# Kernel optimization log

Hardware: AMD Instinct MI355X
Metric: run time of the kernel (lower is better)

Reference implementation:

```python
import jax, jax.numpy as jnp
import numpy as np

N = 50000
E = 400000
D = 128

def _linear(v, W, b):
    return v @ W + b

def setup_inputs() -> dict:
    key = jax.random.key(0)
    ks = jax.random.split(key, 24)
    inp = {
        'h': jax.random.normal(ks[0], (N, D), jnp.float32),
        'x': jax.random.normal(ks[1], (N, 3), jnp.float32),
        'src': jax.random.randint(ks[2], (E,), 0, N, jnp.int32),
        'dst': jax.random.randint(ks[3], (E,), 0, N, jnp.int32),
        'distances': jax.random.uniform(ks[4], (E,), jnp.float32),
        'bpp_bias': jax.random.uniform(ks[5], (E,), jnp.float32),
        'msa_bias': jax.random.uniform(ks[6], (E,), jnp.float32),
        'chem_bias': jax.random.uniform(ks[7], (E,), jnp.float32),
        'relative_offset': jax.random.normal(ks[8], (E,), jnp.float32),
        'chain_break_mask': jax.random.uniform(ks[9], (E,), jnp.float32),
    }
    s = 0.05
    # weights stored [in, out] (transpose of torch Linear)
    inp['msg_W1'] = jax.random.normal(ks[10], (2 * D + 6, D), jnp.float32) * s
    inp['msg_b1'] = jnp.zeros((D,), jnp.float32)
    inp['msg_W2'] = jax.random.normal(ks[11], (D, D), jnp.float32) * s
    inp['msg_b2'] = jnp.zeros((D,), jnp.float32)
    inp['h_W1'] = jax.random.normal(ks[12], (2 * D, D), jnp.float32) * s
    inp['h_b1'] = jnp.zeros((D,), jnp.float32)
    inp['h_W2'] = jax.random.normal(ks[13], (D, D), jnp.float32) * s
    inp['h_b2'] = jnp.zeros((D,), jnp.float32)
    inp['c_W1'] = jax.random.normal(ks[14], (D, D), jnp.float32) * s
    inp['c_b1'] = jnp.zeros((D,), jnp.float32)
    inp['c_W2'] = jax.random.normal(ks[15], (D, 1), jnp.float32) * s
    inp['c_b2'] = jnp.zeros((1,), jnp.float32)
    return inp

def reference(h, x, src, dst, distances, bpp_bias, msa_bias, chem_bias,
              relative_offset, chain_break_mask,
              msg_W1, msg_b1, msg_W2, msg_b2,
              h_W1, h_b1, h_W2, h_b2,
              c_W1, c_b1, c_W2, c_b2):
    n = h.shape[0]
    h_src = h[src]                      # [E, D]
    h_dst = h[dst]                      # [E, D]
    diff = x[src] - x[dst]              # [E, 3]
    dist2 = (distances * distances)[:, None]
    feat = jnp.concatenate([
        h_src, h_dst, dist2,
        bpp_bias[:, None], msa_bias[:, None], chem_bias[:, None],
        relative_offset[:, None], chain_break_mask[:, None]], axis=-1)  # [E, 2D+6]
    m_ij = jax.nn.silu(_linear(jax.nn.silu(_linear(feat, msg_W1, msg_b1)), msg_W2, msg_b2))  # [E, D]
    counts = jax.ops.segment_sum(jnp.ones((src.shape[0],), h.dtype), src, num_segments=n)[:, None]  # [N,1]
    denom = jnp.maximum(counts, 1.0)
    m_i = jax.ops.segment_sum(m_ij, src, num_segments=n) / denom      # [N, D]
    h_out = h + _linear(jax.nn.silu(_linear(jnp.concatenate([h, m_i], -1), h_W1, h_b1)), h_W2, h_b2)
    coef = jnp.tanh(_linear(jax.nn.silu(_linear(m_ij, c_W1, c_b1)), c_W2, c_b2))  # [E, 1]
    delta = jax.ops.segment_sum(diff * coef, src, num_segments=n) / denom          # [N, 3]
    x_out = x + delta
    return h_out, x_out
```

## Files before the change

### kernel.cpp

```cpp
#include <hip/hip_runtime.h>
#include <hip/hip_bf16.h>

typedef short bf16x8 __attribute__((ext_vector_type(8)));
typedef float f32x16 __attribute__((ext_vector_type(16)));
typedef int   i32x4v __attribute__((ext_vector_type(4)));
typedef unsigned u32;

#define MFMA32(a,b,c) __builtin_amdgcn_mfma_f32_32x32x16_bf16((a),(b),(c),0,0,0)

__device__ __forceinline__ u32 pkbf(float x, float y) {
  union { u32 u; __hip_bfloat16 h[2]; } t;
  t.h[0] = __float2bfloat16(x);
  t.h[1] = __float2bfloat16(y);
  return t.u;
}
__device__ __forceinline__ float bf2f(u32 lo16) {
  union { u32 u; float f; } t; t.u = lo16 << 16; return t.f;
}
__device__ __forceinline__ float silu_f(float v) { return v / (1.f + __expf(-v)); }
__device__ __forceinline__ float tanh_f(float v) {
  float e = __expf(2.f * fabsf(v));
  float t = 1.f - 2.f / (e + 1.f);
  return copysignf(t, v);
}

template<int NT>
__device__ __forceinline__ void stage_w128t(const float* __restrict__ W, short* wA, int tid) {
  for (int p = tid; p < 8192; p += NT) {
    int j = p & 127;
    int k = (p >> 7) << 1;
    u32 u = pkbf(W[k * 128 + j], W[k * 128 + 128 + j]);
    int off = j * 256 + (((k >> 3) ^ (j & 15)) << 4) + ((k & 7) << 1);
    *(u32*)((char*)wA + off) = u;
  }
}
__device__ __forceinline__ bf16x8 ldsA(const short* wA, int j, int kbase) {
  int off = j * 256 + (((kbase >> 3) ^ (j & 15)) << 4);
  return __builtin_bit_cast(bf16x8, *(const i32x4v*)((const char*)wA + off));
}

__device__ __forceinline__ void row_chunks(u32 p0, u32 p1, u32 p2, u32 p3,
                                           u32 p4, u32 p5, u32 p6, u32 p7,
                                           int hi, char* rowptr, int jm) {
  u32 x0 = (u32)__shfl_xor((int)(hi ? p0 : p4), 32);
  u32 x1 = (u32)__shfl_xor((int)(hi ? p1 : p5), 32);
  u32 x2 = (u32)__shfl_xor((int)(hi ? p2 : p6), 32);
  u32 x3 = (u32)__shfl_xor((int)(hi ? p3 : p7), 32);
  i32x4v c0, c1;
  if (hi) {
    c0[0] = (int)x0; c0[1] = (int)x1; c0[2] = (int)p4; c0[3] = (int)p5;
    c1[0] = (int)x2; c1[1] = (int)x3; c1[2] = (int)p6; c1[3] = (int)p7;
  } else {
    c0[0] = (int)p0; c0[1] = (int)p1; c0[2] = (int)x0; c0[3] = (int)x1;
    c1[0] = (int)p2; c1[1] = (int)p3; c1[2] = (int)x2; c1[3] = (int)x3;
  }
  *(i32x4v*)(rowptr + jm * 64 + hi * 32)      = c0;
  *(i32x4v*)(rowptr + jm * 64 + hi * 32 + 16) = c1;
}

__device__ __forceinline__ void trans_store1(const f32x16& a, const float* bias, int hi,
                                             char* rowptr, bool va, int jm) {
  float v[16];
  #pragma unroll
  for (int r = 0; r < 16; ++r) {
    int rowloc = (r & 3) + 8 * (r >> 2) + 4 * hi;
    v[r] = silu_f(a[r] + bias[jm * 32 + rowloc]);
  }
  u32 p0 = pkbf(v[0], v[1]),  p1 = pkbf(v[2], v[3]);
  u32 p2 = pkbf(v[4], v[5]),  p3 = pkbf(v[6], v[7]);
  u32 p4 = pkbf(v[8], v[9]),  p5 = pkbf(v[10], v[11]);
  u32 p6 = pkbf(v[12], v[13]), p7 = pkbf(v[14], v[15]);
  if (va) row_chunks(p0, p1, p2, p3, p4, p5, p6, p7, hi, rowptr, jm);
}

__device__ __forceinline__ void trans_frag1(const f32x16& a, const float* bias, int hi,
                                            i32x4v* fr, char* rowptr, bool va, int jm) {
  float v[16];
  #pragma unroll
  for (int r = 0; r < 16; ++r) {
    int rowloc = (r & 3) + 8 * (r >> 2) + 4 * hi;
    v[r] = silu_f(a[r] + bias[jm * 32 + rowloc]);
  }
  u32 p0 = pkbf(v[0], v[1]),  p1 = pkbf(v[2], v[3]);
  u32 p2 = pkbf(v[4], v[5]),  p3 = pkbf(v[6], v[7]);
  u32 p4 = pkbf(v[8], v[9]),  p5 = pkbf(v[10], v[11]);
  u32 p6 = pkbf(v[12], v[13]), p7 = pkbf(v[14], v[15]);
  {
    u32 g1 = (u32)__shfl_xor((int)(hi ? p0 : p2), 32);
    u32 g2 = (u32)__shfl_xor((int)(hi ? p1 : p3), 32);
    i32x4v w;
    w[0] = hi ? (int)g1 : (int)p0;
    w[1] = hi ? (int)g2 : (int)p1;
    w[2] = hi ? (int)p2 : (int)g1;
    w[3] = hi ? (int)p3 : (int)g2;
    fr[jm * 2] = w;
    u32 g1b = (u32)__shfl_xor((int)(hi ? p4 : p6), 32);
    u32 g2b = (u32)__shfl_xor((int)(hi ? p5 : p7), 32);
    i32x4v w2;
    w2[0] = hi ? (int)g1b : (int)p4;
    w2[1] = hi ? (int)g2b : (int)p5;
    w2[2] = hi ? (int)p6 : (int)g1b;
    w2[3] = hi ? (int)p7 : (int)g2b;
    fr[jm * 2 + 1] = w2;
  }
  if (va) row_chunks(p0, p1, p2, p3, p4, p5, p6, p7, hi, rowptr, jm);
}


__global__ void kconv(const float* __restrict__ h, char* __restrict__ hbf, int total16) {
  int i = blockIdx.x * 256 + threadIdx.x;
  if (i >= total16) return;
  const float4* h4 = (const float4*)h;
  float4 a = h4[(size_t)i * 2], b = h4[(size_t)i * 2 + 1];
  i32x4v w;
  w[0] = (int)pkbf(a.x, a.y); w[1] = (int)pkbf(a.z, a.w);
  w[2] = (int)pkbf(b.x, b.y); w[3] = (int)pkbf(b.z, b.w);
  *(i32x4v*)(hbf + (size_t)i * 16) = w;
}

__global__ void khist(const int* __restrict__ src, int* __restrict__ cnt, int E) {
  int e = blockIdx.x * 256 + threadIdx.x;
  if (e < E) atomicAdd(&cnt[src[e]], 1);
}

__global__ void kscan1(const int* __restrict__ cnt, int* __restrict__ part,
                       int* __restrict__ bsums, int N) {
  __shared__ int sh[1024];
  int tid = threadIdx.x, i = blockIdx.x * 1024 + tid;
  int v = (i < N) ? cnt[i] : 0;
  sh[tid] = v; __syncthreads();
  for (int off = 1; off < 1024; off <<= 1) {
    int t = (tid >= off) ? sh[tid - off] : 0;
    __syncthreads();
    sh[tid] += t;
    __syncthreads();
  }
  if (i < N) part[i] = sh[tid] - v;
  if (tid == 1023) bsums[blockIdx.x] = sh[1023];
}

__global__ void kscan2(int* __restrict__ bsums, int nb) {
  __shared__ int sh[64];
  int tid = threadIdx.x;
  int v = (tid < nb) ? bsums[tid] : 0;
  sh[tid] = v; __syncthreads();
  for (int off = 1; off < 64; off <<= 1) {
    int t = (tid >= off) ? sh[tid - off] : 0;
    __syncthreads();
    sh[tid] += t;
    __syncthreads();
  }
  if (tid < nb) bsums[tid] = sh[tid] - v;
}

__global__ void kscan3(const int* __restrict__ bsums, int* __restrict__ part,
                       int* __restrict__ head, int N) {
  int i = blockIdx.x * 1024 + threadIdx.x;
  if (i < N) {
    int v = part[i] + bsums[blockIdx.x];
    part[i] = v;
    head[i] = v;
  }
}

__global__ void kscatter(const int* __restrict__ src, const int* __restrict__ dst,
                         const float* __restrict__ dist, const float* __restrict__ bpp,
                         const float* __restrict__ msa, const float* __restrict__ chem,
                         const float* __restrict__ rel, const float* __restrict__ cbm,
                         int* __restrict__ head, int* __restrict__ rec, int E) {
  int e = blockIdx.x * 256 + threadIdx.x;
  if (e >= E) return;
  int s = src[e];
  int p = atomicAdd(&head[s], 1);
  float q = dist[e];
  i32x4v a;
  a[0] = s;
  a[1] = dst[e];
  a[2] = (int)pkbf(q * q, bpp[e]);
  a[3] = (int)pkbf(msa[e], chem[e]);
  *(i32x4v*)(rec + (size_t)p * 8) = a;
  rec[(size_t)p * 8 + 4] = (int)pkbf(rel[e], cbm[e]);
}

__global__ __launch_bounds__(512, 2)
void kedgeA(const char* __restrict__ hbf, const int* __restrict__ rec,
            const float* __restrict__ mW1, const float* __restrict__ mb1,
            char* __restrict__ t1, int E)
{
  __shared__ short wA0[16384], wA1[16384];
  __shared__ short wE[2048];
  __shared__ float sb1[128];

  const int tid = threadIdx.x, wid = tid >> 6, lane = tid & 63;
  const int col = lane & 31, hi = lane >> 5;

  stage_w128t<512>(mW1, wA0, tid);
  stage_w128t<512>(mW1 + 16384, wA1, tid);
  for (int p = tid; p < 2048; p += 512) {
    int j = p >> 4, kk = p & 15;
    float w = (kk < 6) ? mW1[(256 + kk) * 128 + j] : 0.f;
    wE[j * 16 + kk] = (short)(pkbf(w, 0.f) & 0xffffu);
  }
  if (tid < 128) sb1[tid] = mb1[tid];
  __syncthreads();

  const int T = (E + 31) / 32;
  const int stride = gridDim.x * 8;
  int t = blockIdx.x * 8 + wid;
  if (t >= T) return;

  int p = t * 32 + col;
  int pc = p < E ? p : E - 1;
  i32x4v ra = *(const i32x4v*)(rec + (size_t)pc * 8);
  int ev2 = rec[(size_t)pc * 8 + 4];

  while (t < T) {
    bool va = p < E;
    int s = ra[0], d = ra[1];

    i32x4v bs[8], bd[8];
    #pragma unroll
    for (int kc = 0; kc < 8; ++kc)
      bs[kc] = *(const i32x4v*)(hbf + (size_t)s * 256 + kc * 32 + hi * 16);
    #pragma unroll
    for (int kc = 0; kc < 8; ++kc)
      bd[kc] = *(const i32x4v*)(hbf + (size_t)d * 256 + kc * 32 + hi * 16);

    int tn = t + stride;
    int pn = tn * 32 + col;
    int pcn = pn < E ? pn : E - 1;
    i32x4v nra = *(const i32x4v*)(rec + (size_t)pcn * 8);
    int nev2 = rec[(size_t)pcn * 8 + 4];

    char* rowptr = t1 + (size_t)p * 256;
    #pragma unroll
    for (int g = 0; g < 2; ++g) {
      f32x16 acc2[2];
      #pragma unroll
      for (int j2 = 0; j2 < 2; ++j2)
        #pragma unroll
        for (int r = 0; r < 16; ++r) acc2[j2][r] = 0.f;

      #pragma unroll
      for (int kc = 0; kc < 8; ++kc) {
        bf16x8 bb = __builtin_bit_cast(bf16x8, bs[kc]);
        #pragma unroll
        for (int j2 = 0; j2 < 2; ++j2)
          acc2[j2] = MFMA32(ldsA(wA0, (g * 2 + j2) * 32 + col, kc * 16 + hi * 8), bb, acc2[j2]);
      }
      #pragma unroll
      for (int kc = 0; kc < 8; ++kc) {
        bf16x8 bb = __builtin_bit_cast(bf16x8, bd[kc]);
        #pragma unroll
        for (int j2 = 0; j2 < 2; ++j2)
          acc2[j2] = MFMA32(ldsA(wA1, (g * 2 + j2) * 32 + col, kc * 16 + hi * 8), bb, acc2[j2]);
      }
      {
        i32x4v ev;
        ev[0] = hi ? 0 : ra[2];
        ev[1] = hi ? 0 : ra[3];
        ev[2] = hi ? 0 : ev2;
        ev[3] = 0;
        bf16x8 be = __builtin_bit_cast(bf16x8, ev);
        #pragma unroll
        for (int j2 = 0; j2 < 2; ++j2) {
          bf16x8 af = __builtin_bit_cast(bf16x8,
              *(const i32x4v*)((const char*)wE + ((g * 2 + j2) * 32 + col) * 32 + hi * 16));
          acc2[j2] = MFMA32(af, be, acc2[j2]);
        }
      }
      #pragma unroll
      for (int j2 = 0; j2 < 2; ++j2)
        trans_store1(acc2[j2], sb1, hi, rowptr, va, g * 2 + j2);
    }

    t = tn; p = pn; ra = nra; ev2 = nev2;
  }
}

__global__ __launch_bounds__(512, 2)
void kedgeB(char* buf,
            const float* __restrict__ mW2, const float* __restrict__ mb2,
            const float* __restrict__ cW1, const float* __restrict__ cb1,
            const float* __restrict__ cW2v, const float* __restrict__ cb2,
            float* __restrict__ coef, int E)
{
  __shared__ short wA2[16384], wA3[16384];
  __shared__ float sb2[128], scb1[128], scw2[128];
  __shared__ float scb2v[1];

  const int tid = threadIdx.x, wid = tid >> 6, lane = tid & 63;
  const int col = lane & 31, hi = lane >> 5;

  stage_w128t<512>(mW2, wA2, tid);
  stage_w128t<512>(cW1, wA3, tid);
  if (tid < 128) {
    sb2[tid] = mb2[tid]; scb1[tid] = cb1[tid]; scw2[tid] = cW2v[tid];
  }
  if (tid == 0) scb2v[0] = cb2[0];
  __syncthreads();

  const int T = (E + 31) / 32;
  const int stride = gridDim.x * 8;
  for (int t = blockIdx.x * 8 + wid; t < T; t += stride) {
    int p = t * 32 + col;
    bool va = p < E;
    int pc = va ? p : E - 1;

    i32x4v b[8];
    #pragma unroll
    for (int kc = 0; kc < 8; ++kc)
      b[kc] = *(const i32x4v*)(buf + (size_t)pc * 256 + kc * 32 + hi * 16);

    char* rowptr = buf + (size_t)p * 256;
    i32x4v fr[8];
    #pragma unroll
    for (int g = 0; g < 2; ++g) {
      f32x16 acc2[2];
      #pragma unroll
      for (int j2 = 0; j2 < 2; ++j2)
        #pragma unroll
        for (int r = 0; r < 16; ++r) acc2[j2][r] = 0.f;
      #pragma unroll
      for (int kc = 0; kc < 8; ++kc) {
        bf16x8 bb = __builtin_bit_cast(bf16x8, b[kc]);
        #pragma unroll
        for (int j2 = 0; j2 < 2; ++j2)
          acc2[j2] = MFMA32(ldsA(wA2, (g * 2 + j2) * 32 + col, kc * 16 + hi * 8), bb, acc2[j2]);
      }
      #pragma unroll
      for (int j2 = 0; j2 < 2; ++j2)
        trans_frag1(acc2[j2], sb2, hi, fr, rowptr, va, g * 2 + j2);
    }

    float part = 0.f;
    #pragma unroll
    for (int g = 0; g < 2; ++g) {
      f32x16 acc2[2];
      #pragma unroll
      for (int j2 = 0; j2 < 2; ++j2)
        #pragma unroll
        for (int r = 0; r < 16; ++r) acc2[j2][r] = 0.f;
      #pragma unroll
      for (int kc = 0; kc < 8; ++kc) {
        bf16x8 bb = __builtin_bit_cast(bf16x8, fr[kc]);
        #pragma unroll
        for (int j2 = 0; j2 < 2; ++j2)
          acc2[j2] = MFMA32(ldsA(wA3, (g * 2 + j2) * 32 + col, kc * 16 + hi * 8), bb, acc2[j2]);
      }
      #pragma unroll
      for (int j2 = 0; j2 < 2; ++j2) {
        int jm = g * 2 + j2;
        #pragma unroll
        for (int r = 0; r < 16; ++r) {
          int rowloc = (r & 3) + 8 * (r >> 2) + 4 * hi;
          part += silu_f(acc2[j2][r] + scb1[jm * 32 + rowloc]) * scw2[jm * 32 + rowloc];
        }
      }
    }
    part += __shfl_xor(part, 32);
    float cf = tanh_f(part + scb2v[0]);
    if (va && hi == 0) coef[p] = cf;
  }
}

__global__ __launch_bounds__(256)
void kagg(const char* __restrict__ m_ij, const int* __restrict__ row_start,
          const int* __restrict__ cnt, const float* __restrict__ coef,
          const int* __restrict__ rec, const float* __restrict__ x,
          char* __restrict__ mibf, float* __restrict__ outX, int N)
{
  int n = blockIdx.x * 16 + (threadIdx.x >> 4);
  int t = threadIdx.x & 15;
  if (n >= N) return;
  int st = row_start[n], c = cnt[n];
  float a[8] = {0.f, 0.f, 0.f, 0.f, 0.f, 0.f, 0.f, 0.f};
  for (int k = 0; k < c; ++k) {
    i32x4v u = *(const i32x4v*)(m_ij + (size_t)(st + k) * 256 + t * 16);
    #pragma unroll
    for (int q = 0; q < 4; ++q) {
      u32 w = (u32)u[q];
      a[q * 2]     += bf2f(w & 0xffffu);
      a[q * 2 + 1] += bf2f(w >> 16);
    }
  }
  float inv = 1.f / fmaxf((float)c, 1.f);
  i32x4v o;
  #pragma unroll
  for (int q = 0; q < 4; ++q) o[q] = (int)pkbf(a[q * 2] * inv, a[q * 2 + 1] * inv);
  *(i32x4v*)(mibf + (size_t)n * 256 + t * 16) = o;
  if (t == 0) {
    float x0 = x[(size_t)n * 3], x1 = x[(size_t)n * 3 + 1], x2 = x[(size_t)n * 3 + 2];
    float dx = 0.f, dy = 0.f, dz = 0.f;
    for (int k = 0; k < c; ++k) {
      float cf = coef[st + k];
      int dn = rec[(size_t)(st + k) * 8 + 1];
      dx += (x0 - x[(size_t)dn * 3])     * cf;
      dy += (x1 - x[(size_t)dn * 3 + 1]) * cf;
      dz += (x2 - x[(size_t)dn * 3 + 2]) * cf;
    }
    outX[(size_t)n * 3]     = x0 + dx * inv;
    outX[(size_t)n * 3 + 1] = x1 + dy * inv;
    outX[(size_t)n * 3 + 2] = x2 + dz * inv;
  }
}

__global__ __launch_bounds__(512, 2)
void knode1(const char* __restrict__ hbf, const char* __restrict__ mibf,
            const float* __restrict__ hW1, const float* __restrict__ hb1,
            char* __restrict__ t1h, int N)
{
  __shared__ short wA0[16384], wA1[16384];
  __shared__ float sb1[128];
  const int tid = threadIdx.x, wid = tid >> 6, lane = tid & 63;
  const int col = lane & 31, hi = lane >> 5;
  stage_w128t<512>(hW1, wA0, tid);
  stage_w128t<512>(hW1 + 16384, wA1, tid);
  if (tid < 128) sb1[tid] = hb1[tid];
  __syncthreads();

  int T = (N + 31) / 32;
  int t = blockIdx.x * 8 + wid;
  if (t >= T) return;
  int n = t * 32 + col;
  bool va = n < N;
  int nc = va ? n : N - 1;

  i32x4v bh[8], bm[8];
  #pragma unroll
  for (int kc = 0; kc < 8; ++kc)
    bh[kc] = *(const i32x4v*)(hbf + (size_t)nc * 256 + kc * 32 + hi * 16);
  #pragma unroll
  for (int kc = 0; kc < 8; ++kc)
    bm[kc] = *(const i32x4v*)(mibf + (size_t)nc * 256 + kc * 32 + hi * 16);

  char* rowptr = t1h + (size_t)n * 256;
  #pragma unroll
  for (int g = 0; g < 2; ++g) {
    f32x16 acc2[2];
    #pragma unroll
    for (int j2 = 0; j2 < 2; ++j2)
      #pragma unroll
      for (int r = 0; r < 16; ++r) acc2[j2][r] = 0.f;
    #pragma unroll
    for (int kc = 0; kc < 8; ++kc) {
      bf16x8 bb = __builtin_bit_cast(bf16x8, bh[kc]);
      #pragma unroll
      for (int j2 = 0; j2 < 2; ++j2)
        acc2[j2] = MFMA32(ldsA(wA0, (g * 2 + j2) * 32 + col, kc * 16 + hi * 8), bb, acc2[j2]);
    }
    #pragma unroll
    for (int kc = 0; kc < 8; ++kc) {
      bf16x8 bb = __builtin_bit_cast(bf16x8, bm[kc]);
      #pragma unroll
      for (int j2 = 0; j2 < 2; ++j2)
        acc2[j2] = MFMA32(ldsA(wA1, (g * 2 + j2) * 32 + col, kc * 16 + hi * 8), bb, acc2[j2]);
    }
    #pragma unroll
    for (int j2 = 0; j2 < 2; ++j2)
      trans_store1(acc2[j2], sb1, hi, rowptr, va, g * 2 + j2);
  }
}

__global__ __launch_bounds__(512, 2)
void knode2(const char* __restrict__ t1h, const float* __restrict__ hW2,
            const float* __restrict__ hb2, const float* __restrict__ h,
            float* __restrict__ outH, int N)
{
  __shared__ short wA0[16384];
  __shared__ float sb2[128];
  const int tid = threadIdx.x, wid = tid >> 6, lane = tid & 63;
  const int col = lane & 31, hi = lane >> 5;
  stage_w128t<512>(hW2, wA0, tid);
  if (tid < 128) sb2[tid] = hb2[tid];
  __syncthreads();

  int T = (N + 31) / 32;
  int t = blockIdx.x * 8 + wid;
  if (t >= T) return;
  int n = t * 32 + col;
  bool va = n < N;
  int nc = va ? n : N - 1;

  i32x4v b[8];
  #pragma unroll
  for (int kc = 0; kc < 8; ++kc)
    b[kc] = *(const i32x4v*)(t1h + (size_t)nc * 256 + kc * 32 + hi * 16);

  const float4* h4 = (const float4*)h;
  #pragma unroll
  for (int g = 0; g < 2; ++g) {
    f32x16 acc2[2];
    #pragma unroll
    for (int j2 = 0; j2 < 2; ++j2)
      #pragma unroll
      for (int r = 0; r < 16; ++r) acc2[j2][r] = 0.f;
    #pragma unroll
    for (int kc = 0; kc < 8; ++kc) {
      bf16x8 bb = __builtin_bit_cast(bf16x8, b[kc]);
      #pragma unroll
      for (int j2 = 0; j2 < 2; ++j2)
        acc2[j2] = MFMA32(ldsA(wA0, (g * 2 + j2) * 32 + col, kc * 16 + hi * 8), bb, acc2[j2]);
    }
    #pragma unroll
    for (int j2 = 0; j2 < 2; ++j2) {
      int jm = g * 2 + j2;
      #pragma unroll
      for (int rq = 0; rq < 4; ++rq) {
        int j0 = jm * 32 + rq * 8 + hi * 4;
        float4 hv = h4[(size_t)nc * 32 + (j0 >> 2)];
        float4 o;
        o.x = hv.x + acc2[j2][rq * 4 + 0] + sb2[j0 + 0];
        o.y = hv.y + acc2[j2][rq * 4 + 1] + sb2[j0 + 1];
        o.z = hv.z + acc2[j2][rq * 4 + 2] + sb2[j0 + 2];
        o.w = hv.w + acc2[j2][rq * 4 + 3] + sb2[j0 + 3];
        if (va) ((float4*)outH)[(size_t)nc * 32 + (j0 >> 2)] = o;
      }
    }
  }
}


extern "C" void kernel_launch(void* const* d_in, const int* in_sizes, int n_in,
                              void* d_out, int out_size, void* d_ws, size_t ws_size,
                              hipStream_t stream) {
  const float* h    = (const float*)d_in[0];
  const float* x    = (const float*)d_in[1];
  const int*   src  = (const int*)d_in[2];
  const int*   dst  = (const int*)d_in[3];
  const float* dist = (const float*)d_in[4];
  const float* bpp  = (const float*)d_in[5];
  const float* msa  = (const float*)d_in[6];
  const float* chem = (const float*)d_in[7];
  const float* rel  = (const float*)d_in[8];
  const float* cbm  = (const float*)d_in[9];
  const float* mW1  = (const float*)d_in[10];
  const float* mb1  = (const float*)d_in[11];
  const float* mW2  = (const float*)d_in[12];
  const float* mb2  = (const float*)d_in[13];
  const float* hW1  = (const float*)d_in[14];
  const float* hb1  = (const float*)d_in[15];
  const float* hW2  = (const float*)d_in[16];
  const float* hb2  = (const float*)d_in[17];
  const float* cW1  = (const float*)d_in[18];
  const float* cb1  = (const float*)d_in[19];
  const float* cW2  = (const float*)d_in[20];
  const float* cb2  = (const float*)d_in[21];

  int N = in_sizes[0] / 128;
  int E = in_sizes[2];

  size_t off = 0;
  auto A = [&](size_t b) { size_t o = off; off += (b + 255) & ~(size_t)255; return o; };
  size_t o_cnt  = A((size_t)N * 4);
  size_t o_rs   = A((size_t)N * 4);
  size_t o_head = A((size_t)N * 4);
  size_t o_rec  = A((size_t)E * 32);
  size_t o_coef = A((size_t)E * 4);
  size_t o_bs   = A(1024);
  size_t o_hbf  = A((size_t)N * 256);
  size_t o_mibf = A((size_t)N * 256);
  size_t o_big  = A((size_t)E * 256);

  char* W = (char*)d_ws;
  int*   cnt32 = (int*)(W + o_cnt);
  int*   rs    = (int*)(W + o_rs);
  int*   head  = (int*)(W + o_head);
  int*   rec   = (int*)(W + o_rec);
  float* coef  = (float*)(W + o_coef);
  int*   bsums = (int*)(W + o_bs);
  char*  hbf   = W + o_hbf;
  char*  mibf  = W + o_mibf;
  char*  big   = W + o_big;

  hipMemsetAsync(cnt32, 0, (size_t)N * 4, stream);
  kconv<<<(N * 16 + 255) / 256, 256, 0, stream>>>(h, hbf, N * 16);
  khist<<<(E + 255) / 256, 256, 0, stream>>>(src, cnt32, E);
  int nb = (N + 1023) / 1024;
  kscan1<<<nb, 1024, 0, stream>>>(cnt32, rs, bsums, N);
  kscan2<<<1, 64, 0, stream>>>(bsums, nb);
  kscan3<<<nb, 1024, 0, stream>>>(bsums, rs, head, N);
  kscatter<<<(E + 255) / 256, 256, 0, stream>>>(src, dst, dist, bpp, msa, chem, rel, cbm,
                                                head, rec, E);
  kedgeA<<<512, 512, 0, stream>>>(hbf, rec, mW1, mb1, big, E);
  kedgeB<<<512, 512, 0, stream>>>(big, mW2, mb2, cW1, cb1, cW2, cb2, coef, E);
  kagg<<<(N + 15) / 16, 256, 0, stream>>>(big, rs, cnt32, coef, rec, x,
                                          mibf, (float*)d_out + (size_t)N * 128, N);
  int tb = ((N + 31) / 32 + 7) / 8;
  knode1<<<tb, 512, 0, stream>>>(hbf, mibf, hW1, hb1, big, N);
  knode2<<<tb, 512, 0, stream>>>(big, hW2, hb2, h, (float*)d_out, N);
}
```

Measured before the change: 669.5 us.

## Fuse m_ij segment-sum into edge kernel via segmented wave scan and atomics

The second edge MLP kernel no longer writes m_ij back to the big edge buffer. Instead it does a segmented inclusive scan across the 32 edges in each tile, keyed on the sorted source index, and issues float atomic adds of each segment's partial sum into an fp32 node accumulator. The node aggregation kernel now handles only the coordinate update. The first node kernel normalises the fp32 sums by the edge count and converts them to bf16. This removes the 400k×256B write and re-read of m_ij, at the cost of many shuffles per element, global atomics, an extra memset of N×512B, and non-deterministic fp32 summation order.

New measurement: 748.0 us. 11.7% more time.

```diff
diff --git a/kernel.cpp b/kernel.cpp
--- a/kernel.cpp
+++ b/kernel.cpp
@@ -73,37 +73,27 @@
   if (va) row_chunks(p0, p1, p2, p3, p4, p5, p6, p7, hi, rowptr, jm);
 }
 
-__device__ __forceinline__ void trans_frag1(const f32x16& a, const float* bias, int hi,
-                                            i32x4v* fr, char* rowptr, bool va, int jm) {
-  float v[16];
-  #pragma unroll
-  for (int r = 0; r < 16; ++r) {
-    int rowloc = (r & 3) + 8 * (r >> 2) + 4 * hi;
-    v[r] = silu_f(a[r] + bias[jm * 32 + rowloc]);
-  }
+__device__ __forceinline__ void frags_from_v(const float* v, int hi, i32x4v* fr, int jm) {
   u32 p0 = pkbf(v[0], v[1]),  p1 = pkbf(v[2], v[3]);
   u32 p2 = pkbf(v[4], v[5]),  p3 = pkbf(v[6], v[7]);
   u32 p4 = pkbf(v[8], v[9]),  p5 = pkbf(v[10], v[11]);
   u32 p6 = pkbf(v[12], v[13]), p7 = pkbf(v[14], v[15]);
-  {
-    u32 g1 = (u32)__shfl_xor((int)(hi ? p0 : p2), 32);
-    u32 g2 = (u32)__shfl_xor((int)(hi ? p1 : p3), 32);
-    i32x4v w;
-    w[0] = hi ? (int)g1 : (int)p0;
-    w[1] = hi ? (int)g2 : (int)p1;
-    w[2] = hi ? (int)p2 : (int)g1;
-    w[3] = hi ? (int)p3 : (int)g2;
-    fr[jm * 2] = w;
-    u32 g1b = (u32)__shfl_xor((int)(hi ? p4 : p6), 32);
-    u32 g2b = (u32)__shfl_xor((int)(hi ? p5 : p7), 32);
-    i32x4v w2;
-    w2[0] = hi ? (int)g1b : (int)p4;
-    w2[1] = hi ? (int)g2b : (int)p5;
-    w2[2] = hi ? (int)p6 : (int)g1b;
-    w2[3] = hi ? (int)p7 : (int)g2b;
-    fr[jm * 2 + 1] = w2;
-  }
-  if (va) row_chunks(p0, p1, p2, p3, p4, p5, p6, p7, hi, rowptr, jm);
+  u32 g1 = (u32)__shfl_xor((int)(hi ? p0 : p2), 32);
+  u32 g2 = (u32)__shfl_xor((int)(hi ? p1 : p3), 32);
+  i32x4v w;
+  w[0] = hi ? (int)g1 : (int)p0;
+  w[1] = hi ? (int)g2 : (int)p1;
+  w[2] = hi ? (int)p2 : (int)g1;
+  w[3] = hi ? (int)p3 : (int)g2;
+  fr[jm * 2] = w;
+  u32 g1b = (u32)__shfl_xor((int)(hi ? p4 : p6), 32);
+  u32 g2b = (u32)__shfl_xor((int)(hi ? p5 : p7), 32);
+  i32x4v w2;
+  w2[0] = hi ? (int)g1b : (int)p4;
+  w2[1] = hi ? (int)g2b : (int)p5;
+  w2[2] = hi ? (int)p6 : (int)g1b;
+  w2[3] = hi ? (int)p7 : (int)g2b;
+  fr[jm * 2 + 1] = w2;
 }
 
 
@@ -279,11 +269,11 @@
 }
 
 __global__ __launch_bounds__(512, 2)
-void kedgeB(char* buf,
+void kedgeB(const char* __restrict__ buf, const int* __restrict__ rec,
             const float* __restrict__ mW2, const float* __restrict__ mb2,
             const float* __restrict__ cW1, const float* __restrict__ cb1,
             const float* __restrict__ cW2v, const float* __restrict__ cb2,
-            float* __restrict__ coef, int E)
+            float* __restrict__ m_sum, float* __restrict__ coef, int E)
 {
   __shared__ short wA2[16384], wA3[16384];
   __shared__ float sb2[128], scb1[128], scw2[128];
@@ -307,12 +297,24 @@
     bool va = p < E;
     int pc = va ? p : E - 1;
 
+    int skey = rec[(size_t)pc * 8];
+
     i32x4v b[8];
     #pragma unroll
     for (int kc = 0; kc < 8; ++kc)
       b[kc] = *(const i32x4v*)(buf + (size_t)pc * 256 + kc * 32 + hi * 16);
 
-    char* rowptr = buf + (size_t)p * 256;
+    int nk[5];
+    #pragma unroll
+    for (int st = 0; st < 5; ++st) {
+      int off = 1 << st;
+      int sl = (col >= off) ? (lane - off) : lane;
+      nk[st] = __shfl(skey, sl);
+    }
+    int slT = (col == 31) ? lane : (lane + 1);
+    int keyNext = __shfl(skey, slT);
+    bool tail = (col == 31) || (keyNext != skey);
+
     i32x4v fr[8];
     #pragma unroll
     for (int g = 0; g < 2; ++g) {
@@ -329,8 +331,38 @@
           acc2[j2] = MFMA32(ldsA(wA2, (g * 2 + j2) * 32 + col, kc * 16 + hi * 8), bb, acc2[j2]);
       }
       #pragma unroll
-      for (int j2 = 0; j2 < 2; ++j2)
-        trans_frag1(acc2[j2], sb2, hi, fr, rowptr, va, g * 2 + j2);
+      for (int j2 = 0; j2 < 2; ++j2) {
+        int jm = g * 2 + j2;
+        float v[16];
+        #pragma unroll
+        for (int r = 0; r < 16; ++r) {
+          int rowloc = (r & 3) + 8 * (r >> 2) + 4 * hi;
+          v[r] = silu_f(acc2[j2][r] + sb2[jm * 32 + rowloc]);
+        }
+        frags_from_v(v, hi, fr, jm);
+        if (!va)
+          #pragma unroll
+          for (int r = 0; r < 16; ++r) v[r] = 0.f;
+        #pragma unroll
+        for (int st = 0; st < 5; ++st) {
+          int off = 1 << st;
+          int sl = (col >= off) ? (lane - off) : lane;
+          bool ok = (col >= off) && (nk[st] == skey);
+          #pragma unroll
+          for (int r = 0; r < 16; ++r) {
+            float nv = __shfl(v[r], sl);
+            if (ok) v[r] += nv;
+          }
+        }
+        if (tail) {
+          float* dstp = m_sum + (size_t)skey * 128 + jm * 32;
+          #pragma unroll
+          for (int r = 0; r < 16; ++r) {
+            int rowloc = (r & 3) + 8 * (r >> 2) + 4 * hi;
+            unsafeAtomicAdd(dstp + rowloc, v[r]);
+          }
+        }
+      }
     }
 
     float part = 0.f;
@@ -365,48 +397,31 @@
 }
 
 __global__ __launch_bounds__(256)
-void kagg(const char* __restrict__ m_ij, const int* __restrict__ row_start,
-          const int* __restrict__ cnt, const float* __restrict__ coef,
-          const int* __restrict__ rec, const float* __restrict__ x,
-          char* __restrict__ mibf, float* __restrict__ outX, int N)
+void kaggx(const int* __restrict__ row_start, const int* __restrict__ cnt,
+           const float* __restrict__ coef, const int* __restrict__ rec,
+           const float* __restrict__ x, float* __restrict__ outX, int N)
 {
-  int n = blockIdx.x * 16 + (threadIdx.x >> 4);
-  int t = threadIdx.x & 15;
+  int n = blockIdx.x * 256 + threadIdx.x;
   if (n >= N) return;
   int st = row_start[n], c = cnt[n];
-  float a[8] = {0.f, 0.f, 0.f, 0.f, 0.f, 0.f, 0.f, 0.f};
+  float x0 = x[(size_t)n * 3], x1 = x[(size_t)n * 3 + 1], x2 = x[(size_t)n * 3 + 2];
+  float dx = 0.f, dy = 0.f, dz = 0.f;
   for (int k = 0; k < c; ++k) {
-    i32x4v u = *(const i32x4v*)(m_ij + (size_t)(st + k) * 256 + t * 16);
-    #pragma unroll
-    for (int q = 0; q < 4; ++q) {
-      u32 w = (u32)u[q];
-      a[q * 2]     += bf2f(w & 0xffffu);
-      a[q * 2 + 1] += bf2f(w >> 16);
-    }
+    float cf = coef[st + k];
+    int dn = rec[(size_t)(st + k) * 8 + 1];
+    dx += (x0 - x[(size_t)dn * 3])     * cf;
+    dy += (x1 - x[(size_t)dn * 3 + 1]) * cf;
+    dz += (x2 - x[(size_t)dn * 3 + 2]) * cf;
   }
   float inv = 1.f / fmaxf((float)c, 1.f);
-  i32x4v o;
-  #pragma unroll
-  for (int q = 0; q < 4; ++q) o[q] = (int)pkbf(a[q * 2] * inv, a[q * 2 + 1] * inv);
-  *(i32x4v*)(mibf + (size_t)n * 256 + t * 16) = o;
-  if (t == 0) {
-    float x0 = x[(size_t)n * 3], x1 = x[(size_t)n * 3 + 1], x2 = x[(size_t)n * 3 + 2];
-    float dx = 0.f, dy = 0.f, dz = 0.f;
-    for (int k = 0; k < c; ++k) {
-      float cf = coef[st + k];
-      int dn = rec[(size_t)(st + k) * 8 + 1];
-      dx += (x0 - x[(size_t)dn * 3])     * cf;
-      dy += (x1 - x[(size_t)dn * 3 + 1]) * cf;
-      dz += (x2 - x[(size_t)dn * 3 + 2]) * cf;
-    }
-    outX[(size_t)n * 3]     = x0 + dx * inv;
-    outX[(size_t)n * 3 + 1] = x1 + dy * inv;
-    outX[(size_t)n * 3 + 2] = x2 + dz * inv;
-  }
+  outX[(size_t)n * 3]     = x0 + dx * inv;
+  outX[(size_t)n * 3 + 1] = x1 + dy * inv;
+  outX[(size_t)n * 3 + 2] = x2 + dz * inv;
 }
 
 __global__ __launch_bounds__(512, 2)
-void knode1(const char* __restrict__ hbf, const char* __restrict__ mibf,
+void knode1(const char* __restrict__ hbf, const float* __restrict__ m_sum,
+            const int* __restrict__ cnt,
             const float* __restrict__ hW1, const float* __restrict__ hb1,
             char* __restrict__ t1h, int N)
 {
@@ -425,14 +440,24 @@
   int n = t * 32 + col;
   bool va = n < N;
   int nc = va ? n : N - 1;
+  float inv = 1.f / fmaxf((float)cnt[nc], 1.f);
 
   i32x4v bh[8], bm[8];
   #pragma unroll
   for (int kc = 0; kc < 8; ++kc)
     bh[kc] = *(const i32x4v*)(hbf + (size_t)nc * 256 + kc * 32 + hi * 16);
+  const float4* m4 = (const float4*)m_sum;
   #pragma unroll
-  for (int kc = 0; kc < 8; ++kc)
-    bm[kc] = *(const i32x4v*)(mibf + (size_t)nc * 256 + kc * 32 + hi * 16);
+  for (int kc = 0; kc < 8; ++kc) {
+    float4 a  = m4[(size_t)nc * 32 + kc * 4 + hi * 2 + 0];
+    float4 bq = m4[(size_t)nc * 32 + kc * 4 + hi * 2 + 1];
+    i32x4v w;
+    w[0] = (int)pkbf(a.x * inv, a.y * inv);
+    w[1] = (int)pkbf(a.z * inv, a.w * inv);
+    w[2] = (int)pkbf(bq.x * inv, bq.y * inv);
+    w[3] = (int)pkbf(bq.z * inv, bq.w * inv);
+    bm[kc] = w;
+  }
 
   char* rowptr = t1h + (size_t)n * 256;
   #pragma unroll
@@ -559,7 +584,7 @@
   size_t o_coef = A((size_t)E * 4);
   size_t o_bs   = A(1024);
   size_t o_hbf  = A((size_t)N * 256);
-  size_t o_mibf = A((size_t)N * 256);
+  size_t o_msum = A((size_t)N * 512);
   size_t o_big  = A((size_t)E * 256);
 
   char* W = (char*)d_ws;
@@ -570,10 +595,11 @@
   float* coef  = (float*)(W + o_coef);
   int*   bsums = (int*)(W + o_bs);
   char*  hbf   = W + o_hbf;
-  char*  mibf  = W + o_mibf;
+  float* msum  = (float*)(W + o_msum);
   char*  big   = W + o_big;
 
   hipMemsetAsync(cnt32, 0, (size_t)N * 4, stream);
+  hipMemsetAsync(msum, 0, (size_t)N * 512, stream);
   kconv<<<(N * 16 + 255) / 256, 256, 0, stream>>>(h, hbf, N * 16);
   khist<<<(E + 255) / 256, 256, 0, stream>>>(src, cnt32, E);
   int nb = (N + 1023) / 1024;
@@ -583,10 +609,11 @@
   kscatter<<<(E + 255) / 256, 256, 0, stream>>>(src, dst, dist, bpp, msa, chem, rel, cbm,
                                                 head, rec, E);
   kedgeA<<<512, 512, 0, stream>>>(hbf, rec, mW1, mb1, big, E);
-  kedgeB<<<512, 512, 0, stream>>>(big, mW2, mb2, cW1, cb1, cW2, cb2, coef, E);
-  kagg<<<(N + 15) / 16, 256, 0, stream>>>(big, rs, cnt32, coef, rec, x,
-                                          mibf, (float*)d_out + (size_t)N * 128, N);
+  kedgeB<<<512, 512, 0, stream>>>(big, rec, mW2, mb2, cW1, cb1, cW2, cb2,
+                                  msum, coef, E);
+  kaggx<<<(N + 255) / 256, 256, 0, stream>>>(rs, cnt32, coef, rec, x,
+                                             (float*)d_out + (size_t)N * 128, N);
   int tb = ((N + 31) / 32 + 7) / 8;
-  knode1<<<tb, 512, 0, stream>>>(hbf, mibf, hW1, hb1, big, N);
+  knode1<<<tb, 512, 0, stream>>>(hbf, msum, cnt32, hW1, hb1, big, N);
   knode2<<<tb, 512, 0, stream>>>(big, hW2, hb2, h, (float*)d_out, N);
 }
```
